# Kernel optimization log

Hardware: AMD Instinct MI355X
Metric: run time of the kernel (lower is better)

## Reference

```python
import jax, jax.numpy as jnp
import numpy as np

N_NODES = 100000
N_EDGES = 1600000
D_FEAT = 64


def setup_inputs() -> dict:
    key = jax.random.key(0)
    k1, k2, k3, k4 = jax.random.split(key, 4)
    features = jax.random.normal(k1, (N_NODES, D_FEAT), dtype=jnp.float32)
    edge_weights = jax.random.uniform(k2, (N_EDGES,), dtype=jnp.float32)
    neighbor_idx = jax.random.randint(k3, (N_EDGES,), 0, N_NODES, dtype=jnp.int32)
    segment_ids = jnp.sort(jax.random.randint(k4, (N_EDGES,), 0, N_NODES, dtype=jnp.int32))
    return {"features": features, "edge_weights": edge_weights,
            "neighbor_idx": neighbor_idx, "segment_ids": segment_ids}


def reference(features, edge_weights, neighbor_idx, segment_ids):
    n = features.shape[0]
    # Per-destination-node weight sum and degree.
    wsum = jax.ops.segment_sum(edge_weights, segment_ids, num_segments=n)  # [N]
    deg = jax.ops.segment_sum(jnp.ones_like(edge_weights), segment_ids, num_segments=n)  # [N]
    # If a node's weight sum is 0, fall back to unweighted mean (weight=1, denom=deg).
    use_mean = wsum == 0.0  # [N]
    eff_w = jnp.where(use_mean[segment_ids], 1.0, edge_weights)  # [E]
    gathered = features[neighbor_idx]  # [E, D] gather
    num = jax.ops.segment_sum(eff_w[:, None] * gathered, segment_ids, num_segments=n)  # [N, D]
    den = jnp.where(use_mean, deg, wsum)
    den = jnp.where(den == 0.0, 1.0, den)  # empty nodes -> zeros output
    return num / den[:, None]
```

## Files before the change

kernel.cpp:

```cpp
#include <hip/hip_runtime.h>


#define D_FEAT 64

__global__ __launch_bounds__(256) void WeightedAggregator_28424093564968_kernel(
        const float* __restrict__ feat,
        const float* __restrict__ ew,
        const int*   __restrict__ nidx,
        const int*   __restrict__ seg,
        float*       __restrict__ out,
        int N, int E) {
    const int wave = (blockIdx.x * blockDim.x + threadIdx.x) >> 6;
    const int lane = threadIdx.x & 63;
    if (wave >= N) return;
    const int n = wave;

    int lo = 0, hi = E;
    while (hi - lo > 64) {
        const long long span = hi - lo;
        const int p = lo + (int)((span * (lane + 1)) / 65);
        const bool ge = seg[p] >= n;
        const unsigned long long mask = __ballot(ge);
        if (mask == 0ull) {
            lo = lo + (int)((span * 64) / 65);
        } else {
            const int first = __ffsll((long long)mask) - 1;
            const int nhi = lo + (int)((span * (first + 1)) / 65);
            const int nlo = (first == 0) ? lo : lo + (int)((span * first) / 65);
            lo = nlo; hi = nhi;
        }
    }
    {
        const int p = lo + lane;
        const bool ge = (p >= hi) || (seg[p] >= n);
        const unsigned long long mask = __ballot(ge);
        lo = (mask == 0ull) ? hi : lo + __ffsll((long long)mask) - 1;
    }
    const int start = lo;

    int end = start;
    for (;;) {
        const int p = end + lane;
        const bool stop = (p >= E) || (seg[p] > n);
        const unsigned long long mask = __ballot(stop);
        if (mask) { end += __ffsll((long long)mask) - 1; break; }
        end += 64;
    }

    float ws = 0.0f;
    for (int e = start + lane; e < end; e += 64) ws += ew[e];
    #pragma unroll
    for (int off = 32; off > 0; off >>= 1) ws += __shfl_xor(ws, off);

    const bool  use_mean = (ws == 0.0f);
    const float deg = (float)(end - start);
    float den = use_mean ? deg : ws;
    if (den == 0.0f) den = 1.0f;

    const int slot = lane >> 4;
    const int dofs = (lane & 15) << 2;

    float ax = 0.f, ay = 0.f, az = 0.f, aw = 0.f;
    for (int e = start; e < end; e += 8) {
        const int p0 = e + slot;
        const int p1 = e + 4 + slot;
        const bool v0 = p0 < end;
        const bool v1 = p1 < end;
        const int  i0 = v0 ? nidx[p0] : 0;
        const int  i1 = v1 ? nidx[p1] : 0;
        const float w0 = v0 ? (use_mean ? 1.0f : ew[p0]) : 0.0f;
        const float w1 = v1 ? (use_mean ? 1.0f : ew[p1]) : 0.0f;
        const float4 f0 = *(const float4*)(feat + (size_t)i0 * D_FEAT + dofs);
        const float4 f1 = *(const float4*)(feat + (size_t)i1 * D_FEAT + dofs);
        ax += w0 * f0.x; ay += w0 * f0.y; az += w0 * f0.z; aw += w0 * f0.w;
        ax += w1 * f1.x; ay += w1 * f1.y; az += w1 * f1.z; aw += w1 * f1.w;
    }

    #pragma unroll
    for (int m = 16; m <= 32; m <<= 1) {
        ax += __shfl_xor(ax, m);
        ay += __shfl_xor(ay, m);
        az += __shfl_xor(az, m);
        aw += __shfl_xor(aw, m);
    }

    if (slot == 0) {
        const float inv = 1.0f / den;
        float4 r;
        r.x = ax * inv; r.y = ay * inv; r.z = az * inv; r.w = aw * inv;
        *(float4*)(out + (size_t)n * D_FEAT + dofs) = r;
    }
}

extern "C" void kernel_launch(void* const* d_in, const int* in_sizes, int n_in,
                              void* d_out, int out_size, void* d_ws, size_t ws_size,
                              hipStream_t stream) {
    const float* feat = (const float*)d_in[0];
    const float* ew   = (const float*)d_in[1];
    const int*   nidx = (const int*)d_in[2];
    const int*   seg  = (const int*)d_in[3];
    float*       out  = (float*)d_out;

    const int E = in_sizes[1];
    const int N = in_sizes[0] / D_FEAT;

    const int waves_per_block = 256 / 64;
    const int grid = (N + waves_per_block - 1) / waves_per_block;
    WeightedAggregator_28424093564968_kernel<<<grid, 256, 0, stream>>>(
        feat, ew, nidx, seg, out, N, E);
}
```

Before: 165.9 us.

## Build CSR offsets in a pre-pass and add a degree-64 fast path

Adds a pre-kernel that turns the sorted segment ids into a CSR offset array in workspace memory. The main kernel then reads start and end directly, replacing the per-wave binary search and linear end scan. For nodes of degree at most 64 it loads indices and weights once per lane and broadcasts them with shuffles, avoiding repeated global loads. It costs one extra launch and a pass over the segment ids, and falls back to the search kernel when the workspace is too small.

```diff
diff --git a/kernel.cpp b/kernel.cpp
--- a/kernel.cpp
+++ b/kernel.cpp
@@ -2,14 +2,108 @@
 
 
 #define D_FEAT 64
+
+__global__ __launch_bounds__(256) void WA_build_offsets_kernel(
+        const int* __restrict__ seg, int* __restrict__ offs, int N, int E) {
+    const int tid = blockIdx.x * blockDim.x + threadIdx.x;
+    if (tid > E) return;
+    const int cur  = (tid == E) ? N : seg[tid];
+    const int prev = (tid == 0) ? -1 : seg[tid - 1];
+    for (int v = prev + 1; v <= cur; ++v) offs[v] = tid;
+}
 
 __global__ __launch_bounds__(256) void WeightedAggregator_28424093564968_kernel(
         const float* __restrict__ feat,
         const float* __restrict__ ew,
         const int*   __restrict__ nidx,
-        const int*   __restrict__ seg,
+        const int*   __restrict__ offs,
         float*       __restrict__ out,
-        int N, int E) {
+        int N) {
+    const int wave = (blockIdx.x * blockDim.x + threadIdx.x) >> 6;
+    const int lane = threadIdx.x & 63;
+    if (wave >= N) return;
+    const int n = wave;
+
+    const int start = offs[n];
+    const int end   = offs[n + 1];
+    const int deg   = end - start;
+
+    const int slot = lane >> 4;
+    const int dofs = (lane & 15) << 2;
+
+    float ax = 0.f, ay = 0.f, az = 0.f, aw = 0.f;
+    float den;
+    bool  use_mean;
+
+    if (deg <= 64) {
+        const int  e    = start + lane;
+        const bool vl   = lane < deg;
+        const int  idxl = vl ? nidx[e] : 0;
+        const float wl  = vl ? ew[e]   : 0.0f;
+
+        float ws = wl;
+        #pragma unroll
+        for (int off = 32; off > 0; off >>= 1) ws += __shfl_xor(ws, off);
+        use_mean = (ws == 0.0f);
+        den = use_mean ? (float)deg : ws;
+        if (den == 0.0f) den = 1.0f;
+
+        const int ng = (deg + 3) >> 2;
+        #pragma unroll 4
+        for (int g = 0; g < ng; ++g) {
+            const int  src = (g << 2) + slot;
+            const int  ie  = __shfl(idxl, src);
+            float      we  = __shfl(wl, src);
+            const bool ve  = src < deg;
+            we = ve ? (use_mean ? 1.0f : we) : 0.0f;
+            const float4 f = *(const float4*)(feat + (size_t)ie * D_FEAT + dofs);
+            ax += we * f.x; ay += we * f.y; az += we * f.z; aw += we * f.w;
+        }
+    } else {
+        float ws = 0.0f;
+        for (int e = start + lane; e < end; e += 64) ws += ew[e];
+        #pragma unroll
+        for (int off = 32; off > 0; off >>= 1) ws += __shfl_xor(ws, off);
+        use_mean = (ws == 0.0f);
+        den = use_mean ? (float)deg : ws;
+        if (den == 0.0f) den = 1.0f;
+
+        for (int e = start; e < end; e += 8) {
+            const int p0 = e + slot;
+            const int p1 = e + 4 + slot;
+            const bool v0 = p0 < end;
+            const bool v1 = p1 < end;
+            const int  i0 = v0 ? nidx[p0] : 0;
+            const int  i1 = v1 ? nidx[p1] : 0;
+            const float w0 = v0 ? (use_mean ? 1.0f : ew[p0]) : 0.0f;
+            const float w1 = v1 ? (use_mean ? 1.0f : ew[p1]) : 0.0f;
+            const float4 f0 = *(const float4*)(feat + (size_t)i0 * D_FEAT + dofs);
+            const float4 f1 = *(const float4*)(feat + (size_t)i1 * D_FEAT + dofs);
+            ax += w0 * f0.x; ay += w0 * f0.y; az += w0 * f0.z; aw += w0 * f0.w;
+            ax += w1 * f1.x; ay += w1 * f1.y; az += w1 * f1.z; aw += w1 * f1.w;
+        }
+    }
+
+    #pragma unroll
+    for (int m = 16; m <= 32; m <<= 1) {
+        ax += __shfl_xor(ax, m);
+        ay += __shfl_xor(ay, m);
+        az += __shfl_xor(az, m);
+        aw += __shfl_xor(aw, m);
+    }
+
+    if (slot == 0) {
+        const float inv = 1.0f / den;
+        float4 r;
+        r.x = ax * inv; r.y = ay * inv; r.z = az * inv; r.w = aw * inv;
+        *(float4*)(out + (size_t)n * D_FEAT + dofs) = r;
+    }
+}
+
+__global__ __launch_bounds__(256) void WA_search_kernel(
+        const float* __restrict__ feat, const float* __restrict__ ew,
+        const int* __restrict__ nidx, const int* __restrict__ seg,
+        float* __restrict__ out, int N, int E) {
     const int wave = (blockIdx.x * blockDim.x + threadIdx.x) >> 6;
     const int lane = threadIdx.x & 63;
     if (wave >= N) return;
@@ -37,7 +131,6 @@
         lo = (mask == 0ull) ? hi : lo + __ffsll((long long)mask) - 1;
     }
     const int start = lo;
-
     int end = start;
     for (;;) {
         const int p = end + lane;
@@ -51,21 +144,16 @@
     for (int e = start + lane; e < end; e += 64) ws += ew[e];
     #pragma unroll
     for (int off = 32; off > 0; off >>= 1) ws += __shfl_xor(ws, off);
-
-    const bool  use_mean = (ws == 0.0f);
-    const float deg = (float)(end - start);
-    float den = use_mean ? deg : ws;
+    const bool use_mean = (ws == 0.0f);
+    float den = use_mean ? (float)(end - start) : ws;
     if (den == 0.0f) den = 1.0f;
 
     const int slot = lane >> 4;
     const int dofs = (lane & 15) << 2;
-
     float ax = 0.f, ay = 0.f, az = 0.f, aw = 0.f;
     for (int e = start; e < end; e += 8) {
-        const int p0 = e + slot;
-        const int p1 = e + 4 + slot;
-        const bool v0 = p0 < end;
-        const bool v1 = p1 < end;
+        const int p0 = e + slot, p1 = e + 4 + slot;
+        const bool v0 = p0 < end, v1 = p1 < end;
         const int  i0 = v0 ? nidx[p0] : 0;
         const int  i1 = v1 ? nidx[p1] : 0;
         const float w0 = v0 ? (use_mean ? 1.0f : ew[p0]) : 0.0f;
@@ -75,19 +163,14 @@
         ax += w0 * f0.x; ay += w0 * f0.y; az += w0 * f0.z; aw += w0 * f0.w;
         ax += w1 * f1.x; ay += w1 * f1.y; az += w1 * f1.z; aw += w1 * f1.w;
     }
-
     #pragma unroll
     for (int m = 16; m <= 32; m <<= 1) {
-        ax += __shfl_xor(ax, m);
-        ay += __shfl_xor(ay, m);
-        az += __shfl_xor(az, m);
-        aw += __shfl_xor(aw, m);
-    }
-
+        ax += __shfl_xor(ax, m); ay += __shfl_xor(ay, m);
+        az += __shfl_xor(az, m); aw += __shfl_xor(aw, m);
+    }
     if (slot == 0) {
         const float inv = 1.0f / den;
-        float4 r;
-        r.x = ax * inv; r.y = ay * inv; r.z = az * inv; r.w = aw * inv;
+        float4 r; r.x = ax*inv; r.y = ay*inv; r.z = az*inv; r.w = aw*inv;
         *(float4*)(out + (size_t)n * D_FEAT + dofs) = r;
     }
 }
@@ -106,6 +189,14 @@
 
     const int waves_per_block = 256 / 64;
     const int grid = (N + waves_per_block - 1) / waves_per_block;
-    WeightedAggregator_28424093564968_kernel<<<grid, 256, 0, stream>>>(
-        feat, ew, nidx, seg, out, N, E);
-}
+
+    if (ws_size >= (size_t)(N + 1) * sizeof(int)) {
+        int* offs = (int*)d_ws;
+        const int g1 = (E + 1 + 255) / 256;
+        WA_build_offsets_kernel<<<g1, 256, 0, stream>>>(seg, offs, N, E);
+        WeightedAggregator_28424093564968_kernel<<<grid, 256, 0, stream>>>(
+            feat, ew, nidx, offs, out, N);
+    } else {
+        WA_search_kernel<<<grid, 256, 0, stream>>>(feat, ew, nidx, seg, out, N, E);
+    }
+}
```

Result: faster. 142.8 us (-13.9%).

## Build CSR offsets in a pre-pass and aggregate four nodes per wave

Applied to the files above, without the earlier changes.

Adds a kernel that turns the sorted segment ids into CSR row offsets in workspace, replacing the per-wave binary search and end scan. The main kernel then gives each 16-lane slot its own node (four nodes per wave), computing the weight sum and both weighted and unweighted accumulators in one pass, so no separate weight-sum loop or cross-slot shuffle reduction is needed. This costs an extra launch and extra accumulators, and lanes in a wave diverge when neighbouring nodes have different degrees. The old search kernel is kept as a fallback when workspace is too small.

```diff
diff --git a/kernel.cpp b/kernel.cpp
--- a/kernel.cpp
+++ b/kernel.cpp
@@ -3,13 +3,73 @@
 
 #define D_FEAT 64
 
+__global__ __launch_bounds__(256) void WA_build_offsets_kernel(
+        const int* __restrict__ seg, int* __restrict__ offs, int N, int E) {
+    const int tid = blockIdx.x * blockDim.x + threadIdx.x;
+    if (tid > E) return;
+    const int cur  = (tid == E) ? N : seg[tid];
+    const int prev = (tid == 0) ? -1 : seg[tid - 1];
+    for (int v = prev + 1; v <= cur; ++v) offs[v] = tid;
+}
+
 __global__ __launch_bounds__(256) void WeightedAggregator_28424093564968_kernel(
         const float* __restrict__ feat,
         const float* __restrict__ ew,
         const int*   __restrict__ nidx,
-        const int*   __restrict__ seg,
+        const int*   __restrict__ offs,
         float*       __restrict__ out,
-        int N, int E) {
+        int N) {
+    const int gwave = (blockIdx.x * blockDim.x + threadIdx.x) >> 6;
+    const int lane  = threadIdx.x & 63;
+    const int slot  = lane >> 4;
+    const int dofs  = (lane & 15) << 2;
+
+    const int  n  = gwave * 4 + slot;
+    const bool vn = n < N;
+
+    const int start = vn ? offs[n]     : 0;
+    const int end   = vn ? offs[n + 1] : 0;
+    const int deg   = end - start;
+
+    float ws = 0.0f;
+    float awx = 0.f, awy = 0.f, awz = 0.f, aww = 0.f;
+    float aux = 0.f, auy = 0.f, auz = 0.f, auw = 0.f;
+
+    for (int k = 0; __any(k < deg); k += 4) {
+        #pragma unroll
+        for (int j = 0; j < 4; ++j) {
+            const int  kk = k + j;
+            const bool v  = kk < deg;
+            const int  e  = v ? (start + kk) : 0;
+            const int  id = v ? nidx[e] : 0;
+            const float w = v ? ew[e]   : 0.0f;
+            const float s = v ? 1.0f    : 0.0f;
+            const float4 f = *(const float4*)(feat + (size_t)id * D_FEAT + dofs);
+            ws  += w;
+            awx += w * f.x; awy += w * f.y; awz += w * f.z; aww += w * f.w;
+            aux += s * f.x; auy += s * f.y; auz += s * f.z; auw += s * f.w;
+        }
+    }
+
+    const bool use_mean = (ws == 0.0f);
+    float den = use_mean ? (float)deg : ws;
+    if (den == 0.0f) den = 1.0f;
+    const float inv = 1.0f / den;
+
+    if (vn) {
+        float4 r;
+        r.x = (use_mean ? aux : awx) * inv;
+        r.y = (use_mean ? auy : awy) * inv;
+        r.z = (use_mean ? auz : awz) * inv;
+        r.w = (use_mean ? auw : aww) * inv;
+        *(float4*)(out + (size_t)n * D_FEAT + dofs) = r;
+    }
+}
+
+__global__ __launch_bounds__(256) void WA_search_kernel(
+        const float* __restrict__ feat, const float* __restrict__ ew,
+        const int* __restrict__ nidx, const int* __restrict__ seg,
+        float* __restrict__ out, int N, int E) {
     const int wave = (blockIdx.x * blockDim.x + threadIdx.x) >> 6;
     const int lane = threadIdx.x & 63;
     if (wave >= N) return;
@@ -37,7 +97,6 @@
         lo = (mask == 0ull) ? hi : lo + __ffsll((long long)mask) - 1;
     }
     const int start = lo;
-
     int end = start;
     for (;;) {
         const int p = end + lane;
@@ -51,21 +110,16 @@
     for (int e = start + lane; e < end; e += 64) ws += ew[e];
     #pragma unroll
     for (int off = 32; off > 0; off >>= 1) ws += __shfl_xor(ws, off);
-
-    const bool  use_mean = (ws == 0.0f);
-    const float deg = (float)(end - start);
-    float den = use_mean ? deg : ws;
+    const bool use_mean = (ws == 0.0f);
+    float den = use_mean ? (float)(end - start) : ws;
     if (den == 0.0f) den = 1.0f;
 
     const int slot = lane >> 4;
     const int dofs = (lane & 15) << 2;
-
     float ax = 0.f, ay = 0.f, az = 0.f, aw = 0.f;
     for (int e = start; e < end; e += 8) {
-        const int p0 = e + slot;
-        const int p1 = e + 4 + slot;
-        const bool v0 = p0 < end;
-        const bool v1 = p1 < end;
+        const int p0 = e + slot, p1 = e + 4 + slot;
+        const bool v0 = p0 < end, v1 = p1 < end;
         const int  i0 = v0 ? nidx[p0] : 0;
         const int  i1 = v1 ? nidx[p1] : 0;
         const float w0 = v0 ? (use_mean ? 1.0f : ew[p0]) : 0.0f;
@@ -75,19 +129,14 @@
         ax += w0 * f0.x; ay += w0 * f0.y; az += w0 * f0.z; aw += w0 * f0.w;
         ax += w1 * f1.x; ay += w1 * f1.y; az += w1 * f1.z; aw += w1 * f1.w;
     }
-
     #pragma unroll
     for (int m = 16; m <= 32; m <<= 1) {
-        ax += __shfl_xor(ax, m);
-        ay += __shfl_xor(ay, m);
-        az += __shfl_xor(az, m);
-        aw += __shfl_xor(aw, m);
+        ax += __shfl_xor(ax, m); ay += __shfl_xor(ay, m);
+        az += __shfl_xor(az, m); aw += __shfl_xor(aw, m);
     }
-
     if (slot == 0) {
         const float inv = 1.0f / den;
-        float4 r;
-        r.x = ax * inv; r.y = ay * inv; r.z = az * inv; r.w = aw * inv;
+        float4 r; r.x = ax*inv; r.y = ay*inv; r.z = az*inv; r.w = aw*inv;
         *(float4*)(out + (size_t)n * D_FEAT + dofs) = r;
     }
 }
@@ -104,8 +153,16 @@
     const int E = in_sizes[1];
     const int N = in_sizes[0] / D_FEAT;
 
-    const int waves_per_block = 256 / 64;
-    const int grid = (N + waves_per_block - 1) / waves_per_block;
-    WeightedAggregator_28424093564968_kernel<<<grid, 256, 0, stream>>>(
-        feat, ew, nidx, seg, out, N, E);
+    if (ws_size >= (size_t)(N + 1) * sizeof(int)) {
+        int* offs = (int*)d_ws;
+        const int g1 = (E + 1 + 255) / 256;
+        WA_build_offsets_kernel<<<g1, 256, 0, stream>>>(seg, offs, N, E);
+        const int nodes_per_block = 16;
+        const int grid = (N + nodes_per_block - 1) / nodes_per_block;
+        WeightedAggregator_28424093564968_kernel<<<grid, 256, 0, stream>>>(
+            feat, ew, nidx, offs, out, N);
+    } else {
+        const int grid = (N + 3) / 4;
+        WA_search_kernel<<<grid, 256, 0, stream>>>(feat, ew, nidx, seg, out, N, E);
+    }
 }
```

Measured after the change: 147.1 us. 11.4% less time.
